# Optimization experiments

Hardware: AMD Instinct MI355X
Metric: run time of the kernel (lower is better)

The kernel has to match this reference:

```python
import jax, jax.numpy as jnp
import numpy as np
import math

HIDDEN = 768
HEADS = 12
HEAD_DIM = HIDDEN // HEADS


def setup_inputs() -> dict:
    key = jax.random.key(0)
    ks = jax.random.split(key, 8)
    B, N1, N2, H = 2, 2048, 2048, HIDDEN
    s1 = jax.random.normal(ks[0], (B, N1, H), dtype=jnp.float32)
    s2 = jax.random.normal(ks[1], (B, N2, H), dtype=jnp.float32)
    mask = jnp.zeros((B, 1, 1, N2), dtype=jnp.float32)  # additive extended mask
    std = 0.02
    Wq = jax.random.normal(ks[2], (H, H), dtype=jnp.float32) * std
    Wk = jax.random.normal(ks[3], (H, H), dtype=jnp.float32) * std
    Wv = jax.random.normal(ks[4], (H, H), dtype=jnp.float32) * std
    bq = jnp.zeros((H,), jnp.float32)
    bk = jnp.zeros((H,), jnp.float32)
    bv = jnp.zeros((H,), jnp.float32)
    return {"s1_hidden_states": s1, "s2_hidden_states": s2,
            "s2_attention_mask": mask,
            "Wq": Wq, "bq": bq, "Wk": Wk, "bk": bk, "Wv": Wv, "bv": bv}


def _split_heads(x):
    # [B, N, H] -> [B, h, N, d]
    B, N, _ = x.shape
    return x.reshape(B, N, HEADS, HEAD_DIM).transpose(0, 2, 1, 3)


def reference(s1_hidden_states, s2_hidden_states, s2_attention_mask,
              Wq, bq, Wk, bk, Wv, bv):
    q = _split_heads(s1_hidden_states @ Wq + bq)   # [B,h,N1,d]
    k = _split_heads(s2_hidden_states @ Wk + bk)   # [B,h,N2,d]
    v = _split_heads(s2_hidden_states @ Wv + bv)   # [B,h,N2,d]
    scores = jnp.einsum('bhqd,bhkd->bhqk', q, k) / math.sqrt(HEAD_DIM)
    scores = scores + s2_attention_mask            # broadcast [B,1,1,N2]
    probs = jax.nn.softmax(scores, axis=-1)        # [B,h,N1,N2]
    ctx = jnp.einsum('bhqk,bhkd->bhqd', probs, v)  # dropout p=0 (eval)
    B, h, N1, d = ctx.shape
    ctx = ctx.transpose(0, 2, 1, 3).reshape(B, N1, h * d)  # [B,N1,H]
    attn_weights = jnp.sum(probs, axis=1) / HEADS           # [B,N1,N2]
    return ctx, attn_weights
```

## Files before the change

kernel.cpp:

```cpp
#include <hip/hip_runtime.h>
#include <stdint.h>


typedef __attribute__((ext_vector_type(8))) short bf16x8;
typedef __attribute__((ext_vector_type(4))) short bf16x4;
typedef __attribute__((ext_vector_type(4))) float f32x4;

constexpr int B_  = 2;
constexpr int N_  = 2048;
constexpr int HID = 768;
constexpr int NH  = 12;
constexpr int HD  = 64;
constexpr int NSPLIT = 2;
constexpr int KSPAN  = N_ / NSPLIT;
constexpr int NT     = KSPAN / 64;
constexpr float L2E = 1.4426950408889634f;

__device__ __forceinline__ short f2bf(float f) {
    uint32_t u = __builtin_bit_cast(uint32_t, f);
    u = (u + 0x7fffu + ((u >> 16) & 1u)) >> 16;
    return (short)u;
}

__device__ __forceinline__ void gload16(const void* g, void* l) {
    __builtin_amdgcn_global_load_lds(
        (const __attribute__((address_space(1))) unsigned int*)g,
        (__attribute__((address_space(3))) unsigned int*)l, 16, 0, 0);
}

__global__ __launch_bounds__(256) void prep_x(
    const float* __restrict__ s1, const float* __restrict__ s2,
    const float* __restrict__ mask,
    short* __restrict__ X1, short* __restrict__ X2, float* __restrict__ mks)
{
    const int PT = (B_ * N_ * HID) / 4;
    if (blockIdx.x >= 6144) {
        const int idx = (blockIdx.x - 6144) * 256 + threadIdx.x;
        const float4 mv = *reinterpret_cast<const float4*>(&mask[idx * 4]);
        *reinterpret_cast<float4*>(&mks[idx * 4]) =
            make_float4(mv.x * L2E, mv.y * L2E, mv.z * L2E, mv.w * L2E);
        return;
    }
    int i = blockIdx.x * 256 + threadIdx.x;
    const float* S; short* X;
    if (i < PT) { S = s1; X = X1; } else { S = s2; X = X2; i -= PT; }
    const int e   = i * 4;
    const int row = e / HID;
    const int col = e - row * HID;
    const float4 v = *reinterpret_cast<const float4*>(&S[e]);
    float vs[4] = {v.x, v.y, v.z, v.w};
    short4 hi, lo;
    short* hp = &hi.x; short* lp = &lo.x;
    #pragma unroll
    for (int j = 0; j < 4; ++j) {
        const uint32_t u = __builtin_bit_cast(uint32_t, vs[j]);
        hp[j] = (short)(u >> 16);
        const float hif = __builtin_bit_cast(float, u & 0xffff0000u);
        lp[j] = f2bf(vs[j] - hif);
    }
    short* dst = X + (size_t)row * 1536 + col;
    *reinterpret_cast<short4*>(dst)       = hi;
    *reinterpret_cast<short4*>(dst + 768) = lo;
}

__global__ __launch_bounds__(256) void prep_w(
    const float* __restrict__ Wq, const float* __restrict__ Wk,
    const float* __restrict__ Wv, short* __restrict__ WT)
{
    const int z = blockIdx.z;
    const float* W = (z == 0) ? Wq : (z == 1) ? Wk : Wv;
    short* O = WT + (size_t)z * HID * HID;
    __shared__ short Tl[64][66];
    const int k0 = blockIdx.x * 64, n0 = blockIdx.y * 64;
    const int t = threadIdx.x;
    const int rr = t >> 4, cc = (t & 15) * 4;
    #pragma unroll
    for (int i = 0; i < 4; ++i) {
        const int row = i * 16 + rr;
        const float4 w = *reinterpret_cast<const float4*>(&W[(size_t)(k0 + row) * HID + n0 + cc]);
        Tl[cc + 0][row] = f2bf(w.x);
        Tl[cc + 1][row] = f2bf(w.y);
        Tl[cc + 2][row] = f2bf(w.z);
        Tl[cc + 3][row] = f2bf(w.w);
    }
    __syncthreads();
    #pragma unroll
    for (int i = 0; i < 4; ++i) {
        const int n = i * 16 + rr;
        short4 o;
        o.x = Tl[n][cc + 0]; o.y = Tl[n][cc + 1];
        o.z = Tl[n][cc + 2]; o.w = Tl[n][cc + 3];
        *reinterpret_cast<short4*>(&O[(size_t)(n0 + n) * HID + k0 + cc]) = o;
    }
}

__global__ __launch_bounds__(256) void proj_mfma(
    const short* __restrict__ X1, const short* __restrict__ X2,
    const short* __restrict__ WT,
    const float* __restrict__ bq, const float* __restrict__ bk,
    const float* __restrict__ bv,
    short* __restrict__ qb, short* __restrict__ kbm, short* __restrict__ vtb)
{
    const int which = blockIdx.z;
    const char* Xb = (const char*)((which == 0) ? X1 : X2);
    const char* Wb = (const char*)(WT + (size_t)which * HID * HID);
    const float* bias = (which == 0) ? bq : (which == 1) ? bk : bv;
    const int m0 = blockIdx.x * 128;
    const int n0 = blockIdx.y * 128;
    const int t = threadIdx.x;
    const int lane = t & 63;
    const int lg = lane >> 4, lm = lane & 15;
    const int wave = __builtin_amdgcn_readfirstlane(t >> 6);
    const int wr = wave >> 1, wc = wave & 1;

    __shared__ __align__(16) char Ls[32768];
    char* Al = Ls;
    char* Bl = Ls + 16384;

    const int KSTEPS = (which == 2) ? 12 : 24;

    f32x4 acc[4][4];
    #pragma unroll
    for (int mt = 0; mt < 4; ++mt)
        #pragma unroll
        for (int nt = 0; nt < 4; ++nt) acc[mt][nt] = f32x4{0.f, 0.f, 0.f, 0.f};

    auto stage = [&](int ks) {
        const int ka = ks * 128;
        const int kw = (ks % 12) * 128;
        #pragma unroll
        for (int u = 0; u < 4; ++u) {
            const int c = u * 256 + wave * 64 + lane;
            const int row = c >> 3, j = c & 7;
            gload16(Xb + (size_t)(m0 + row) * 3072 + ka + ((j ^ (row & 7)) << 4),
                    Al + u * 4096 + wave * 1024);
        }
        #pragma unroll
        for (int u = 0; u < 4; ++u) {
            const int c = u * 256 + wave * 64 + lane;
            const int row = c >> 3, j = c & 7;
            gload16(Wb + (size_t)(n0 + row) * 1536 + kw + ((j ^ (row & 7)) << 4),
                    Bl + u * 4096 + wave * 1024);
        }
    };

    for (int ks = 0; ks < KSTEPS; ++ks) {
        stage(ks);
        __syncthreads();
        #pragma unroll
        for (int ksub = 0; ksub < 2; ++ksub) {
            const int jj = ksub * 4 + lg;
            bf16x8 a[4], bb[4];
            #pragma unroll
            for (int mt = 0; mt < 4; ++mt) {
                const int r = wr * 64 + mt * 16 + lm;
                a[mt] = *reinterpret_cast<const bf16x8*>(
                    Al + (r << 7) + ((jj ^ (r & 7)) << 4));
            }
            #pragma unroll
            for (int nt = 0; nt < 4; ++nt) {
                const int r = wc * 64 + nt * 16 + lm;
                bb[nt] = *reinterpret_cast<const bf16x8*>(
                    Bl + (r << 7) + ((jj ^ (r & 7)) << 4));
            }
            __builtin_amdgcn_s_setprio(1);
            #pragma unroll
            for (int mt = 0; mt < 4; ++mt)
                #pragma unroll
                for (int nt = 0; nt < 4; ++nt)
                    acc[mt][nt] = __builtin_amdgcn_mfma_f32_16x16x32_bf16(
                        a[mt], bb[nt], acc[mt][nt], 0, 0, 0);
            __builtin_amdgcn_s_setprio(0);
        }
        __syncthreads();
    }

    const int b = m0 >> 11;

    if (which != 2) {
        const float sc = (which == 0) ? (0.125f * L2E) : 1.0f;
        short* dst = (which == 0) ? qb : kbm;
        const int head = blockIdx.y * 2 + wc;
        const size_t bh = (size_t)(b * NH + head);
        #pragma unroll
        for (int mt = 0; mt < 4; ++mt)
            #pragma unroll
            for (int nt = 0; nt < 4; ++nt) {
                const int d = nt * 16 + lm;
                const float bi = bias[n0 + wc * 64 + d];
                #pragma unroll
                for (int r = 0; r < 4; ++r) {
                    const int mrow = m0 + wr * 64 + mt * 16 + 4 * lg + r;
                    const int n = mrow & 2047;
                    dst[(bh * N_ + n) * HD + d] = f2bf((acc[mt][nt][r] + bi) * sc);
                }
            }
    } else {
        short* Ct = (short*)Ls;
        #pragma unroll
        for (int mt = 0; mt < 4; ++mt)
            #pragma unroll
            for (int nt = 0; nt < 4; ++nt) {
                const int dd = wc * 64 + nt * 16 + lm;
                const float bi = bias[n0 + dd];
                #pragma unroll
                for (int r = 0; r < 4; ++r) {
                    const int ml = wr * 64 + mt * 16 + 4 * lg + r;
                    Ct[dd * 128 + ml] = f2bf(acc[mt][nt][r] + bi);
                }
            }
        __syncthreads();
        const int dd = t >> 1, seg = t & 1;
        const int head = (n0 + dd) >> 6;
        const int d = dd & 63;
        const short* src = Ct + dd * 128 + seg * 64;
        short* dv = vtb + ((size_t)(b * NH + head) * HD + d) * N_ + (m0 & 2047) + seg * 64;
        #pragma unroll
        for (int u = 0; u < 8; ++u)
            *reinterpret_cast<int4*>(dv + u * 8) = *reinterpret_cast<const int4*>(src + u * 8);
    }
}

__global__ __launch_bounds__(256) void flash_kernel(
    const short* __restrict__ qb, const short* __restrict__ kbm,
    const short* __restrict__ vtb, const float* __restrict__ mks,
    float* __restrict__ ctx0, float* __restrict__ ctx1,
    float* __restrict__ l_part)
{
    const int qt = blockIdx.x, h = blockIdx.y;
    const int b = blockIdx.z / NSPLIT, s = blockIdx.z % NSPLIT;
    const int t = threadIdx.x;
    const int lane = t & 63;
    const int wave = __builtin_amdgcn_readfirstlane(t >> 6);
    const int lg = lane >> 4, lm = lane & 15;
    const int q0 = qt * 64 + wave * 16;
    const int kstart = s * KSPAN;

    __shared__ __align__(16) char Kl[2][8192];
    __shared__ __align__(16) char Vl[2][8192];

    const size_t bh = (size_t)(b * NH + h);
    const short* qp  = qb  + (bh * N_ + q0) * HD;
    const char*  kpb = (const char*)(kbm + bh * N_ * HD);
    const char*  vpb = (const char*)(vtb + bh * HD * N_);
    const float* mk  = mks + (size_t)b * N_;

    const bf16x8 qf0 = *reinterpret_cast<const bf16x8*>(qp + lm * HD + lg * 8);
    const bf16x8 qf1 = *reinterpret_cast<const bf16x8*>(qp + lm * HD + lg * 8 + 32);

    bf16x4 onesf;
    onesf[0] = (short)0x3F80; onesf[1] = (short)0x3F80;
    onesf[2] = (short)0x3F80; onesf[3] = (short)0x3F80;

    f32x4 cacc[4];
    #pragma unroll
    for (int vt = 0; vt < 4; ++vt) cacc[vt] = f32x4{0.f, 0.f, 0.f, 0.f};
    f32x4 lacc = f32x4{0.f, 0.f, 0.f, 0.f};
    bf16x4 pa_prev[4];

    auto stageK = [&](int buf, int krow) {
        #pragma unroll
        for (int u = 0; u < 2; ++u) {
            const int c = u * 256 + wave * 64 + lane;
            const int row = c >> 3, j = c & 7;
            gload16(kpb + (size_t)(krow + row) * 128 + ((j ^ (row & 7)) << 4),
                    &Kl[buf][u * 4096 + wave * 1024]);
        }
    };
    auto stageV = [&](int buf, int k0v) {
        #pragma unroll
        for (int u = 0; u < 2; ++u) {
            const int c = u * 256 + wave * 64 + lane;
            const int row = c >> 3, j = c & 7;
            gload16(vpb + (size_t)row * (N_ * 2) + (size_t)k0v * 2
                        + ((j ^ (row & 7)) << 4),
                    &Vl[buf][u * 4096 + wave * 1024]);
        }
    };

    stageK(0, kstart);
    __syncthreads();

    for (int it = 0; it < NT; ++it) {
        const int k0  = kstart + it * 64;
        const int cur = it & 1;
        const bool more = (it + 1 < NT);

        if (more) stageK(cur ^ 1, k0 + 64);
        stageV(cur, k0);

        f32x4 mv4[4];
        #pragma unroll
        for (int kt = 0; kt < 4; ++kt)
            mv4[kt] = *reinterpret_cast<const f32x4*>(&mk[k0 + kt * 16 + 4 * lg]);

        const char* Kb = Kl[cur];
        f32x4 accs[4];
        __builtin_amdgcn_s_setprio(1);
        #pragma unroll
        for (int kt = 0; kt < 4; ++kt) {
            const int r = kt * 16 + lm;
            const bf16x8 kf0 = *reinterpret_cast<const bf16x8*>(
                Kb + (r << 7) + ((lg ^ (r & 7)) << 4));
            const bf16x8 kf1 = *reinterpret_cast<const bf16x8*>(
                Kb + (r << 7) + (((lg + 4) ^ (r & 7)) << 4));
            f32x4 z = mv4[kt];
            z = __builtin_amdgcn_mfma_f32_16x16x32_bf16(kf0, qf0, z, 0, 0, 0);
            z = __builtin_amdgcn_mfma_f32_16x16x32_bf16(kf1, qf1, z, 0, 0, 0);
            accs[kt] = z;
        }
        __builtin_amdgcn_s_setprio(0);

        if (it > 0) {
            const char* Vb = Vl[cur ^ 1];
            __builtin_amdgcn_s_setprio(1);
            #pragma unroll
            for (int kt = 0; kt < 4; ++kt) {
                const int jj = 2 * kt + (lg >> 1);
                #pragma unroll
                for (int vt = 0; vt < 4; ++vt) {
                    const int row = vt * 16 + lm;
                    const bf16x4 vfr = *reinterpret_cast<const bf16x4*>(
                        Vb + (row << 7) + ((jj ^ (row & 7)) << 4) + ((lg & 1) << 3));
                    cacc[vt] = __builtin_amdgcn_mfma_f32_16x16x16bf16_1k(
                        pa_prev[kt], vfr, cacc[vt], 0, 0, 0);
                }
                lacc = __builtin_amdgcn_mfma_f32_16x16x16bf16_1k(
                    pa_prev[kt], onesf, lacc, 0, 0, 0);
            }
            __builtin_amdgcn_s_setprio(0);
        }

        #pragma unroll
        for (int kt = 0; kt < 4; ++kt) {
            const float p0 = exp2f(accs[kt][0]);
            const float p1 = exp2f(accs[kt][1]);
            const float p2 = exp2f(accs[kt][2]);
            const float p3 = exp2f(accs[kt][3]);
            uint32_t u01, u23;
            asm("v_cvt_pk_bf16_f32 %0, %1, %2" : "=v"(u01) : "v"(p0), "v"(p1));
            asm("v_cvt_pk_bf16_f32 %0, %1, %2" : "=v"(u23) : "v"(p2), "v"(p3));
            uint2 u2; u2.x = u01; u2.y = u23;
            pa_prev[kt] = __builtin_bit_cast(bf16x4, u2);
        }

        __syncthreads();
    }

    {
        const char* Vb = Vl[(NT - 1) & 1];
        #pragma unroll
        for (int kt = 0; kt < 4; ++kt) {
            const int jj = 2 * kt + (lg >> 1);
            #pragma unroll
            for (int vt = 0; vt < 4; ++vt) {
                const int row = vt * 16 + lm;
                const bf16x4 vfr = *reinterpret_cast<const bf16x4*>(
                    Vb + (row << 7) + ((jj ^ (row & 7)) << 4) + ((lg & 1) << 3));
                cacc[vt] = __builtin_amdgcn_mfma_f32_16x16x16bf16_1k(
                    pa_prev[kt], vfr, cacc[vt], 0, 0, 0);
            }
            lacc = __builtin_amdgcn_mfma_f32_16x16x16bf16_1k(
                pa_prev[kt], onesf, lacc, 0, 0, 0);
        }
    }

    float* ctxp = (s == 0) ? ctx0 : ctx1;
    #pragma unroll
    for (int r = 0; r < 4; ++r) {
        float* orow = ctxp + ((size_t)b * N_ + q0 + lg * 4 + r) * HID + h * HD;
        #pragma unroll
        for (int vt = 0; vt < 4; ++vt) orow[vt * 16 + lm] = cacc[vt][r];
    }
    if (lm == 0) {
        const size_t idx = (size_t)s * (B_ * NH * N_) + bh * N_ + q0 + lg * 4;
        #pragma unroll
        for (int r = 0; r < 4; ++r) l_part[idx + r] = lacc[r];
    }
}

__global__ __launch_bounds__(256) void merge_kernel(
    float* __restrict__ ctx0, const float* __restrict__ ctx1,
    const float* __restrict__ l_part, float* __restrict__ l_ws)
{
    const int gid  = blockIdx.x * 256 + threadIdx.x;
    const int row  = gid >> 6;
    const int lane = gid & 63;
    const int bh = row >> 11;
    const int n  = row & 2047;
    const int b  = bh / NH, h = bh % NH;
    constexpr int PS = B_ * NH * N_;

    const float L = l_part[row] + l_part[PS + row];
    const float invL = 1.f / L;

    const size_t cidx = ((size_t)b * N_ + n) * HID + h * HD + lane;
    ctx0[cidx] = (ctx0[cidx] + ctx1[cidx]) * invL;

    if (lane == 0) l_ws[row] = invL;
}

__global__ __launch_bounds__(256) void attnw_kernel(
    const short* __restrict__ qb, const short* __restrict__ kbm,
    const float* __restrict__ mks, const float* __restrict__ l_ws,
    float* __restrict__ out_attn)
{
    const int qt = blockIdx.x, ct = blockIdx.y, b = blockIdx.z;
    const int t = threadIdx.x;
    const int lane = t & 63;
    const int wave = __builtin_amdgcn_readfirstlane(t >> 6);
    const int lg = lane >> 4, lm = lane & 15;
    const int q0 = qt * 64 + wave * 16;
    const int kbase = ct * 64;

    __shared__ __align__(16) char Kl[2][8192];
    __shared__ __align__(16) char Ql[2][8192];

    float mv[4];
    #pragma unroll
    for (int kt = 0; kt < 4; ++kt) mv[kt] = mks[(size_t)b * N_ + kbase + kt * 16 + lm];

    f32x4 accw[4];
    #pragma unroll
    for (int kt = 0; kt < 4; ++kt) accw[kt] = f32x4{0.f, 0.f, 0.f, 0.f};

    auto stageK = [&](int buf, int h) {
        const char* kpb = (const char*)(kbm + ((size_t)(b * NH + h) * N_) * HD);
        #pragma unroll
        for (int u = 0; u < 2; ++u) {
            const int c = u * 256 + wave * 64 + lane;
            const int row = c >> 3, j = c & 7;
            gload16(kpb + (size_t)(kbase + row) * 128 + ((j ^ (row & 7)) << 4),
                    &Kl[buf][u * 4096 + wave * 1024]);
        }
    };
    auto stageQ = [&](int buf, int h) {
        const char* qpb = (const char*)(qb + ((size_t)(b * NH + h) * N_ + qt * 64) * HD);
        #pragma unroll
        for (int u = 0; u < 2; ++u) {
            const int c = u * 256 + wave * 64 + lane;
            const int row = c >> 3, j = c & 7;
            gload16(qpb + (size_t)row * 128 + ((j ^ (row & 7)) << 4),
                    &Ql[buf][u * 4096 + wave * 1024]);
        }
    };

    stageK(0, 0);
    stageQ(0, 0);
    __syncthreads();

    for (int h = 0; h < NH; ++h) {
        const bool more = (h + 1 < NH);
        if (more) {
            stageK((h + 1) & 1, h + 1);
            stageQ((h + 1) & 1, h + 1);
        }

        const size_t bh = (size_t)(b * NH + h);
        const char* Qb = Ql[h & 1];
        const int rq = wave * 16 + lm;
        const bf16x8 qf0 = *reinterpret_cast<const bf16x8*>(
            Qb + (rq << 7) + ((lg ^ (rq & 7)) << 4));
        const bf16x8 qf1 = *reinterpret_cast<const bf16x8*>(
            Qb + (rq << 7) + (((lg + 4) ^ (rq & 7)) << 4));
        float il[4];
        #pragma unroll
        for (int r = 0; r < 4; ++r)
            il[r] = l_ws[bh * N_ + q0 + lg * 4 + r];
        const char* Kb = Kl[h & 1];
        __builtin_amdgcn_s_setprio(1);
        #pragma unroll
        for (int kt = 0; kt < 4; ++kt) {
            const int r = kt * 16 + lm;
            const bf16x8 kf0 = *reinterpret_cast<const bf16x8*>(
                Kb + (r << 7) + ((lg ^ (r & 7)) << 4));
            const bf16x8 kf1 = *reinterpret_cast<const bf16x8*>(
                Kb + (r << 7) + (((lg + 4) ^ (r & 7)) << 4));
            f32x4 z = f32x4{0.f, 0.f, 0.f, 0.f};
            z = __builtin_amdgcn_mfma_f32_16x16x32_bf16(qf0, kf0, z, 0, 0, 0);
            z = __builtin_amdgcn_mfma_f32_16x16x32_bf16(qf1, kf1, z, 0, 0, 0);
            #pragma unroll
            for (int rr = 0; rr < 4; ++rr)
                accw[kt][rr] += exp2f(z[rr] + mv[kt]) * il[rr];
        }
        __builtin_amdgcn_s_setprio(0);

        __syncthreads();
    }

    #pragma unroll
    for (int kt = 0; kt < 4; ++kt)
        #pragma unroll
        for (int r = 0; r < 4; ++r)
            out_attn[((size_t)b * N_ + q0 + lg * 4 + r) * N_ + kbase + kt * 16 + lm]
                = accw[kt][r] * (1.0f / 12.0f);
}

extern "C" void kernel_launch(void* const* d_in, const int* in_sizes, int n_in,
                              void* d_out, int out_size, void* d_ws, size_t ws_size,
                              hipStream_t stream) {
    (void)in_sizes; (void)n_in; (void)out_size;
    const float* s1   = (const float*)d_in[0];
    const float* s2   = (const float*)d_in[1];
    const float* mask = (const float*)d_in[2];
    const float* Wq   = (const float*)d_in[3];
    const float* bq   = (const float*)d_in[4];
    const float* Wk   = (const float*)d_in[5];
    const float* bk   = (const float*)d_in[6];
    const float* Wv   = (const float*)d_in[7];
    const float* bv   = (const float*)d_in[8];

    float* out_ctx  = (float*)d_out;
    float* out_attn = out_ctx + (size_t)B_ * N_ * HID;

    const size_t xlen = (size_t)B_ * N_ * 1536;
    const size_t qkv  = (size_t)B_ * NH * N_ * HD;
    const size_t rows = (size_t)B_ * NH * N_;
    short* X1   = (short*)d_ws;
    short* X2   = X1 + xlen;
    short* WT   = X2 + xlen;
    short* qb   = WT + (size_t)3 * HID * HID;
    short* kbm  = qb + qkv;
    short* vtb  = kbm + qkv;
    float* ctx1 = (float*)(vtb + qkv);
    float* l_part = ctx1 + (size_t)B_ * N_ * HID;
    float* l_ws   = l_part + NSPLIT * rows;
    float* mks    = l_ws + rows;
    const size_t need = (size_t)((char*)(mks + (size_t)B_ * N_) - (char*)d_ws);
    if (ws_size < need) return;

    prep_x<<<6148, 256, 0, stream>>>(s1, s2, mask, X1, X2, mks);
    prep_w<<<dim3(12, 12, 3), 256, 0, stream>>>(Wq, Wk, Wv, WT);
    proj_mfma<<<dim3(32, 6, 3), 256, 0, stream>>>(X1, X2, WT, bq, bk, bv, qb, kbm, vtb);
    flash_kernel<<<dim3(N_ / 64, NH, B_ * NSPLIT), 256, 0, stream>>>(
        qb, kbm, vtb, mks, out_ctx, ctx1, l_part);
    merge_kernel<<<(B_ * N_ * HID) / 256, 256, 0, stream>>>(
        out_ctx, ctx1, l_part, l_ws);
    attnw_kernel<<<dim3(N_ / 64, N_ / 64, B_), 256, 0, stream>>>(
        qb, kbm, mks, l_ws, out_attn);
}
```

Before: 155.4 us.

## Remove key-split in flash kernel and fold merge normalization into epilogue

The flash attention kernel now processes the full key range per block instead of splitting it in two. The separate merge kernel and its partial context and partial-sum buffers go away. Normalization by the row sum and the write of the inverse sum are done directly in the flash epilogue. This removes a kernel launch and the extra global traffic for partial context buffers, at the cost of halving the grid size and doubling per-block serial work.

```diff
diff --git a/kernel.cpp b/kernel.cpp
--- a/kernel.cpp
+++ b/kernel.cpp
@@ -11,9 +11,7 @@
 constexpr int HID = 768;
 constexpr int NH  = 12;
 constexpr int HD  = 64;
-constexpr int NSPLIT = 2;
-constexpr int KSPAN  = N_ / NSPLIT;
-constexpr int NT     = KSPAN / 64;
+constexpr int NT  = N_ / 64;
 constexpr float L2E = 1.4426950408889634f;
 
 __device__ __forceinline__ short f2bf(float f) {
@@ -224,17 +222,14 @@
 __global__ __launch_bounds__(256) void flash_kernel(
     const short* __restrict__ qb, const short* __restrict__ kbm,
     const short* __restrict__ vtb, const float* __restrict__ mks,
-    float* __restrict__ ctx0, float* __restrict__ ctx1,
-    float* __restrict__ l_part)
+    float* __restrict__ out_ctx, float* __restrict__ l_ws)
 {
-    const int qt = blockIdx.x, h = blockIdx.y;
-    const int b = blockIdx.z / NSPLIT, s = blockIdx.z % NSPLIT;
+    const int qt = blockIdx.x, h = blockIdx.y, b = blockIdx.z;
     const int t = threadIdx.x;
     const int lane = t & 63;
     const int wave = __builtin_amdgcn_readfirstlane(t >> 6);
     const int lg = lane >> 4, lm = lane & 15;
     const int q0 = qt * 64 + wave * 16;
-    const int kstart = s * KSPAN;
 
     __shared__ __align__(16) char Kl[2][8192];
     __shared__ __align__(16) char Vl[2][8192];
@@ -278,11 +273,11 @@
         }
     };
 
-    stageK(0, kstart);
+    stageK(0, 0);
     __syncthreads();
 
     for (int it = 0; it < NT; ++it) {
-        const int k0  = kstart + it * 64;
+        const int k0  = it * 64;
         const int cur = it & 1;
         const bool more = (it + 1 < NT);
 
@@ -365,39 +360,21 @@
         }
     }
 
-    float* ctxp = (s == 0) ? ctx0 : ctx1;
+    float invl[4];
+    #pragma unroll
+    for (int r = 0; r < 4; ++r) invl[r] = 1.f / lacc[r];
+
     #pragma unroll
     for (int r = 0; r < 4; ++r) {
-        float* orow = ctxp + ((size_t)b * N_ + q0 + lg * 4 + r) * HID + h * HD;
-        #pragma unroll
-        for (int vt = 0; vt < 4; ++vt) orow[vt * 16 + lm] = cacc[vt][r];
+        float* orow = out_ctx + ((size_t)b * N_ + q0 + lg * 4 + r) * HID + h * HD;
+        #pragma unroll
+        for (int vt = 0; vt < 4; ++vt) orow[vt * 16 + lm] = cacc[vt][r] * invl[r];
     }
     if (lm == 0) {
-        const size_t idx = (size_t)s * (B_ * NH * N_) + bh * N_ + q0 + lg * 4;
-        #pragma unroll
-        for (int r = 0; r < 4; ++r) l_part[idx + r] = lacc[r];
-    }
-}
-
-__global__ __launch_bounds__(256) void merge_kernel(
-    float* __restrict__ ctx0, const float* __restrict__ ctx1,
-    const float* __restrict__ l_part, float* __restrict__ l_ws)
-{
-    const int gid  = blockIdx.x * 256 + threadIdx.x;
-    const int row  = gid >> 6;
-    const int lane = gid & 63;
-    const int bh = row >> 11;
-    const int n  = row & 2047;
-    const int b  = bh / NH, h = bh % NH;
-    constexpr int PS = B_ * NH * N_;
-
-    const float L = l_part[row] + l_part[PS + row];
-    const float invL = 1.f / L;
-
-    const size_t cidx = ((size_t)b * N_ + n) * HID + h * HD + lane;
-    ctx0[cidx] = (ctx0[cidx] + ctx1[cidx]) * invL;
-
-    if (lane == 0) l_ws[row] = invL;
+        const size_t idx = bh * N_ + q0 + lg * 4;
+        #pragma unroll
+        for (int r = 0; r < 4; ++r) l_ws[idx + r] = invl[r];
+    }
 }
 
 __global__ __launch_bounds__(256) void attnw_kernel(
@@ -522,20 +499,16 @@
     short* qb   = WT + (size_t)3 * HID * HID;
     short* kbm  = qb + qkv;
     short* vtb  = kbm + qkv;
-    float* ctx1 = (float*)(vtb + qkv);
-    float* l_part = ctx1 + (size_t)B_ * N_ * HID;
-    float* l_ws   = l_part + NSPLIT * rows;
-    float* mks    = l_ws + rows;
+    float* l_ws = (float*)(vtb + qkv);
+    float* mks  = l_ws + rows;
     const size_t need = (size_t)((char*)(mks + (size_t)B_ * N_) - (char*)d_ws);
     if (ws_size < need) return;
 
     prep_x<<<6148, 256, 0, stream>>>(s1, s2, mask, X1, X2, mks);
     prep_w<<<dim3(12, 12, 3), 256, 0, stream>>>(Wq, Wk, Wv, WT);
     proj_mfma<<<dim3(32, 6, 3), 256, 0, stream>>>(X1, X2, WT, bq, bk, bv, qb, kbm, vtb);
-    flash_kernel<<<dim3(N_ / 64, NH, B_ * NSPLIT), 256, 0, stream>>>(
-        qb, kbm, vtb, mks, out_ctx, ctx1, l_part);
-    merge_kernel<<<(B_ * N_ * HID) / 256, 256, 0, stream>>>(
-        out_ctx, ctx1, l_part, l_ws);
+    flash_kernel<<<dim3(N_ / 64, NH, B_), 256, 0, stream>>>(
+        qb, kbm, vtb, mks, out_ctx, l_ws);
     attnw_kernel<<<dim3(N_ / 64, N_ / 64, B_), 256, 0, stream>>>(
         qb, kbm, mks, l_ws, out_attn);
 }
```

After: 144.4 us. 1.08x faster.
